# Kernel optimization log

Hardware: AMD Instinct MI355X
Metric: run time of the kernel (lower is better)

The kernel has to match this reference:

```python
import jax, jax.numpy as jnp
import numpy as np

WINDOW = 5  # window_size from init
C_COARSE = 256
C_FINE = 128


def _gather_windows(fine_nchw, b, lin_idx, stride, pad, w, wc):
    """Extract [M, w*w, C] windows centered on coarse grid cells.

    Equivalent to F.unfold(kernel=w, stride=stride, padding=pad) followed by
    rearrange('n (c ww) l -> n l ww c') and fancy-indexing [b, lin_idx],
    but gathers only the matched windows.
    """
    x = jnp.pad(fine_nchw, ((0, 0), (0, 0), (pad, pad), (pad, pad)))
    x = jnp.transpose(x, (0, 2, 3, 1))  # [N, Hp, Wp, C]
    r = lin_idx // wc
    c = lin_idx % wc
    offs = jnp.arange(w)
    rows = r[:, None] * stride + offs  # [M, w] (start = r*stride - pad, +pad shift)
    cols = c[:, None] * stride + offs  # [M, w]
    patches = x[b[:, None, None], rows[:, :, None], cols[:, None, :]]  # [M, w, w, C]
    return patches.reshape(patches.shape[0], w * w, patches.shape[-1])


def setup_inputs() -> dict:
    key = jax.random.key(0)
    ks = jax.random.split(key, 10)
    N, Hc, Hf, M = 2, 60, 240, 3000
    inp = {
        "coarse_image_feature_1": jax.random.normal(ks[0], (N, Hc * Hc, C_COARSE), jnp.float32),
        "coarse_image_feature_2": jax.random.normal(ks[1], (N, Hc * Hc, C_COARSE), jnp.float32),
        "fine_image_feature_1": jax.random.normal(ks[2], (N, C_FINE, Hf, Hf), jnp.float32),
        "fine_image_feature_2": jax.random.normal(ks[3], (N, C_FINE, Hf, Hf), jnp.float32),
        "batch_indices": jax.random.randint(ks[4], (M,), 0, N),
        "row_indices": jax.random.randint(ks[5], (M,), 0, Hc * Hc),
        "column_indices": jax.random.randint(ks[6], (M,), 0, Hc * Hc),
        "fine_height_width": Hf,
        "coarse_height_width": Hc,
        # learned params (kaiming-normal-ish weights, zero biases)
        "W_dp": jax.random.normal(ks[7], (C_FINE, C_COARSE), jnp.float32) * np.sqrt(2.0 / C_FINE),
        "b_dp": jnp.zeros((C_FINE,), jnp.float32),
        "W_merge": jax.random.normal(ks[8], (C_FINE, 2 * C_FINE), jnp.float32) * np.sqrt(2.0 / C_FINE),
        "b_merge": jnp.zeros((C_FINE,), jnp.float32),
    }
    return inp


def reference(coarse_image_feature_1, coarse_image_feature_2,
              fine_image_feature_1, fine_image_feature_2,
              batch_indices, row_indices, column_indices,
              fine_height_width, coarse_height_width,
              W_dp, b_dp, W_merge, b_merge):
    stride = fine_height_width // coarse_height_width
    pad = WINDOW // 2
    M = batch_indices.shape[0]

    f1 = _gather_windows(fine_image_feature_1, batch_indices, row_indices,
                         stride, pad, WINDOW, coarse_height_width)       # [M, ww, Cf]
    f2 = _gather_windows(fine_image_feature_2, batch_indices, column_indices,
                         stride, pad, WINDOW, coarse_height_width)       # [M, ww, Cf]

    coarse = jnp.concatenate([
        coarse_image_feature_1[batch_indices, row_indices],
        coarse_image_feature_2[batch_indices, column_indices],
    ], axis=0)                                                           # [2M, Cc]
    coarse = coarse @ W_dp.T + b_dp                                      # [2M, Cf]

    fine = jnp.concatenate([f1, f2], axis=0)                             # [2M, ww, Cf]
    combined = jnp.concatenate(
        [fine, jnp.broadcast_to(coarse[:, None, :], fine.shape)], axis=-1)  # [2M, ww, 2Cf]
    merged = combined @ W_merge.T + b_merge                              # [2M, ww, Cf]
    return merged[:M], merged[M:]
```

## Files before the change

kernel.cpp:

```cpp
#include <hip/hip_runtime.h>

#define HF 240
#define HC 60
#define STRIDEF 4
#define PADW 2
#define WIN 5
#define CC 256
#define CF 128
#define NPOS 25
#define NPX (HF*HF)
#define MPB 16
#define TPX 128

typedef __bf16 bf16x8 __attribute__((ext_vector_type(8)));
typedef __bf16 bf16x4 __attribute__((ext_vector_type(4)));
typedef float  f32x4  __attribute__((ext_vector_type(4)));

__global__ void k_prep(const float* __restrict__ W_dp, const float* __restrict__ b_dp,
                       const float* __restrict__ W_merge, const float* __restrict__ b_merge,
                       __bf16* __restrict__ Wm1h, float* __restrict__ W_effT,
                       float* __restrict__ b_eff) {
    const int j = blockIdx.x;
    const int k = threadIdx.x;
    const float* wm2 = W_merge + (size_t)j * (2 * CF) + CF;

    float acc = 0.f, accb = 0.f;
    for (int q = 0; q < CF; ++q) {
        const float wq = wm2[q];
        acc  += wq * W_dp[(size_t)q * CC + k];
        accb += wq * b_dp[q];
    }
    W_effT[(size_t)k * CF + j] = acc;

    if (k < CF)
        Wm1h[(size_t)j * CF + k] = (__bf16)W_merge[(size_t)j * (2 * CF) + k];
    if (k == 0)
        b_eff[j] = accb + b_merge[j];
}

__global__ void k_coarse(const float* __restrict__ c1, const float* __restrict__ c2,
                         const int* __restrict__ bidx, const int* __restrict__ ridx,
                         const int* __restrict__ cidx, int M,
                         const float* __restrict__ W_effT, const float* __restrict__ b_eff,
                         float* __restrict__ c_all) {
    const int m0 = blockIdx.x * MPB;
    const int j  = threadIdx.x;
    const int twoM = 2 * M;
    __shared__ float v[MPB * CC];

    const int nm = (twoM - m0) < MPB ? (twoM - m0) : MPB;
    for (int mm = 0; mm < nm; ++mm) {
        int m = m0 + mm;
        const float* src;
        if (m < M) src = c1 + ((size_t)bidx[m] * (HC * HC) + ridx[m]) * CC;
        else       src = c2 + ((size_t)bidx[m - M] * (HC * HC) + cidx[m - M]) * CC;
        v[mm * CC + j]      = src[j];
        v[mm * CC + j + CF] = src[j + CF];
    }
    __syncthreads();

    float acc[MPB];
    const float be = b_eff[j];
    #pragma unroll
    for (int mm = 0; mm < MPB; ++mm) acc[mm] = be;

    for (int k = 0; k < CC; k += 4) {
        float w0 = W_effT[(k + 0) * CF + j];
        float w1 = W_effT[(k + 1) * CF + j];
        float w2 = W_effT[(k + 2) * CF + j];
        float w3 = W_effT[(k + 3) * CF + j];
        #pragma unroll
        for (int mm = 0; mm < MPB; ++mm) {
            const f32x4 vv = *(const f32x4*)&v[mm * CC + k];
            acc[mm] += w0 * vv.x + w1 * vv.y + w2 * vv.z + w3 * vv.w;
        }
    }
    for (int mm = 0; mm < nm; ++mm)
        c_all[(size_t)(m0 + mm) * CF + j] = acc[mm];
}

__global__ __launch_bounds__(256, 4) void k_tgemm(
    const float* __restrict__ f1, const float* __restrict__ f2,
    const __bf16* __restrict__ Wm1h, __bf16* __restrict__ V) {

    const int slot = blockIdx.y;
    const float* src = (slot >= 2 ? f2 : f1) + (size_t)(slot & 1) * CF * NPX;
    const int px0 = blockIdx.x * TPX;
    const int t  = threadIdx.x;
    const int l  = t & 63;
    const int w  = t >> 6;
    const int lo16 = l & 15;
    const int hi   = l >> 4;

    __shared__ __attribute__((aligned(16))) float chkf[2][32 * TPX];

    const int seg = l >> 5;
    const int q4  = (l & 31) * 4;

#define STAGE(c, b)                                                           \
    {                                                                         \
        _Pragma("unroll")                                                     \
        for (int ii = 0; ii < 4; ++ii) {                                      \
            const int i   = w * 4 + ii;                                       \
            const int chl = 2 * i + seg;                                      \
            const int ch  = (c) * 32 + chl;                                   \
            const int pxg = q4 ^ (((ch >> 3) & 3) << 4);                      \
            const float* gp = src + (size_t)ch * NPX + px0 + pxg;             \
            __builtin_amdgcn_global_load_lds(                                 \
                (const __attribute__((address_space(1))) void*)gp,            \
                (__attribute__((address_space(3))) void*)&chkf[b][i * 256],   \
                16, 0, 0);                                                    \
        }                                                                     \
    }

    f32x4 acc[8][2];
    #pragma unroll
    for (int mt = 0; mt < 8; ++mt) {
        acc[mt][0] = (f32x4){0.f, 0.f, 0.f, 0.f};
        acc[mt][1] = (f32x4){0.f, 0.f, 0.f, 0.f};
    }

    STAGE(0, 0);

    #pragma unroll
    for (int c = 0; c < 4; ++c) {
        const int b = c & 1;
        if (c < 3) STAGE(c + 1, b ^ 1);
        __syncthreads();

        const bf16x8 bf0 = *reinterpret_cast<const bf16x8*>(
            Wm1h + (size_t)(w * 32 + 2 * lo16 + 0) * CF + c * 32 + hi * 8);
        const bf16x8 bf1 = *reinterpret_cast<const bf16x8*>(
            Wm1h + (size_t)(w * 32 + 2 * lo16 + 1) * CF + c * 32 + hi * 8);

        #pragma unroll
        for (int mt = 0; mt < 8; ++mt) {
            const int pxr = (mt * 16 + lo16) ^ (hi << 4);
            bf16x8 a;
            #pragma unroll
            for (int e = 0; e < 8; ++e)
                a[e] = (__bf16)chkf[b][(hi * 8 + e) * TPX + pxr];
            acc[mt][0] = __builtin_amdgcn_mfma_f32_16x16x32_bf16(a, bf0, acc[mt][0], 0, 0, 0);
            acc[mt][1] = __builtin_amdgcn_mfma_f32_16x16x32_bf16(a, bf1, acc[mt][1], 0, 0, 0);
        }
        __syncthreads();
    }
#undef STAGE

    uint* Vp = (uint*)(V + ((size_t)slot * NPX + px0) * CF);
    const int dcol = w * 16 + lo16;
    #pragma unroll
    for (int mt = 0; mt < 8; ++mt) {
        #pragma unroll
        for (int reg = 0; reg < 4; ++reg) {
            const int px = mt * 16 + hi * 4 + reg;
            union { uint u; __bf16 h[2]; } cv;
            cv.h[0] = (__bf16)acc[mt][0][reg];
            cv.h[1] = (__bf16)acc[mt][1][reg];
            Vp[(size_t)px * 64 + dcol] = cv.u;
        }
    }
}

__global__ __launch_bounds__(256) void k_gather(
    const __bf16* __restrict__ V,
    const int* __restrict__ bidx, const int* __restrict__ ridx,
    const int* __restrict__ cidx, int M,
    const float* __restrict__ c_all, float* __restrict__ out) {

    const int m = blockIdx.x;
    const int t = threadIdx.x;
    const int g  = t >> 5;
    const int l32 = t & 31;

    int b, lin, ii;
    if (m < M) { ii = 0; b = bidx[m];     lin = ridx[m]; }
    else       { ii = 1; b = bidx[m - M]; lin = cidx[m - M]; }
    const int slot = ii * 2 + b;
    const int r  = lin / HC, c = lin - r * HC;
    const int y0 = r * STRIDEF - PADW;
    const int x0 = c * STRIDEF - PADW;

    const f32x4 c4 = *reinterpret_cast<const f32x4*>(c_all + (size_t)m * CF + l32 * 4);
    const __bf16* Vb = V + (size_t)slot * NPX * CF;
    float* ob = out + (size_t)m * (NPOS * CF) + l32 * 4;

    #pragma unroll
    for (int pass = 0; pass < 4; ++pass) {
        const int p = pass * 8 + g;
        if (p < NPOS) {
            const int wy = (p * 13) >> 6;
            const int wx = p - wy * WIN;
            const int y = y0 + wy, x = x0 + wx;
            f32x4 o = c4;
            if (y >= 0 && x >= 0) {
                const bf16x4 v = *reinterpret_cast<const bf16x4*>(Vb + (size_t)(y * HF + x) * CF + l32 * 4);
                o.x += (float)v.x; o.y += (float)v.y; o.z += (float)v.z; o.w += (float)v.w;
            }
            __builtin_nontemporal_store(o, reinterpret_cast<f32x4*>(ob + (size_t)p * CF));
        }
    }
}

__global__ __launch_bounds__(256) void k_main_direct(
    const float* __restrict__ f1, const float* __restrict__ f2,
    const int* __restrict__ bidx, const int* __restrict__ ridx,
    const int* __restrict__ cidx, int M,
    const __bf16* __restrict__ Wm1h, const float* __restrict__ c_all,
    float* __restrict__ out) {

    const int m = blockIdx.x;
    const int t = threadIdx.x;
    const int l    = t & 63;
    const int wv   = t >> 6;
    const int lo16 = l & 15;
    const int hi   = l >> 4;

    __shared__ __bf16 patch[32 * CF];

    bf16x8 bfrag[2][4];
    #pragma unroll
    for (int nt2 = 0; nt2 < 2; ++nt2) {
        const int j = wv * 32 + nt2 * 16 + lo16;
        #pragma unroll
        for (int kt = 0; kt < 4; ++kt)
            bfrag[nt2][kt] = *reinterpret_cast<const bf16x8*>(Wm1h + (size_t)j * CF + kt * 32 + hi * 8);
    }

    const float* img; int b, lin;
    if (m < M) { img = f1; b = bidx[m];     lin = ridx[m]; }
    else       { img = f2; b = bidx[m - M]; lin = cidx[m - M]; }
    const int r  = lin / HC, c = lin - r * HC;
    const int y0 = r * STRIDEF - PADW;
    const int x0 = c * STRIDEF - PADW;

    for (int task = t; task < CF * WIN; task += 256) {
        const int ch = task / WIN;
        const int wy = task - ch * WIN;
        const int y  = y0 + wy;
        const bool yok = (y >= 0);
        const float* rowp = img + (((size_t)b * CF + ch) * HF + (yok ? y : 0)) * HF;
        #pragma unroll
        for (int wx = 0; wx < WIN; ++wx) {
            const int x = x0 + wx;
            const float val = (yok && x >= 0) ? rowp[x] : 0.f;
            const int pos = wy * WIN + wx;
            patch[pos * CF + (ch ^ ((pos & 7) << 3))] = (__bf16)val;
        }
    }
    __syncthreads();

    f32x4 acc[2][2];
    #pragma unroll
    for (int mt = 0; mt < 2; ++mt)
        #pragma unroll
        for (int nt2 = 0; nt2 < 2; ++nt2)
            acc[mt][nt2] = (f32x4){0.f, 0.f, 0.f, 0.f};

    const int swz = (lo16 & 7) << 3;
    #pragma unroll
    for (int kt = 0; kt < 4; ++kt) {
        const int koff = (kt * 32 + hi * 8) ^ swz;
        bf16x8 a0 = *reinterpret_cast<const bf16x8*>(&patch[ lo16       * CF + koff]);
        bf16x8 a1 = *reinterpret_cast<const bf16x8*>(&patch[(16 + lo16) * CF + koff]);
        #pragma unroll
        for (int nt2 = 0; nt2 < 2; ++nt2) {
            acc[0][nt2] = __builtin_amdgcn_mfma_f32_16x16x32_bf16(a0, bfrag[nt2][kt], acc[0][nt2], 0, 0, 0);
            acc[1][nt2] = __builtin_amdgcn_mfma_f32_16x16x32_bf16(a1, bfrag[nt2][kt], acc[1][nt2], 0, 0, 0);
        }
    }

    float* ob = out + (size_t)m * (NPOS * CF);
    #pragma unroll
    for (int nt2 = 0; nt2 < 2; ++nt2) {
        const int j  = wv * 32 + nt2 * 16 + lo16;
        const float cv = c_all[(size_t)m * CF + j];
        #pragma unroll
        for (int mt = 0; mt < 2; ++mt) {
            #pragma unroll
            for (int reg = 0; reg < 4; ++reg) {
                const int p = mt * 16 + hi * 4 + reg;
                if (p < NPOS)
                    ob[(size_t)p * CF + j] = acc[mt][nt2][reg] + cv;
            }
        }
    }
}

extern "C" void kernel_launch(void* const* d_in, const int* in_sizes, int n_in,
                              void* d_out, int out_size, void* d_ws, size_t ws_size,
                              hipStream_t stream) {
    const float* c1      = (const float*)d_in[0];
    const float* c2      = (const float*)d_in[1];
    const float* f1      = (const float*)d_in[2];
    const float* f2      = (const float*)d_in[3];
    const int*   bidx    = (const int*)d_in[4];
    const int*   ridx    = (const int*)d_in[5];
    const int*   cidx    = (const int*)d_in[6];
    const float* W_dp    = (const float*)d_in[9];
    const float* b_dp    = (const float*)d_in[10];
    const float* W_merge = (const float*)d_in[11];
    const float* b_merge = (const float*)d_in[12];
    const int M = in_sizes[4];

    char* ws = (char*)d_ws;
    __bf16* Wm1h  = (__bf16*)(ws);
    float* W_effT = (float*)(ws + (64 << 10));
    float* b_eff  = (float*)(ws + (192 << 10));
    float* c_all  = (float*)(ws + (256 << 10));
    __bf16* V     = (__bf16*)(ws + (4 << 20));

    const size_t need_V = (size_t)(4 << 20) + (size_t)4 * NPX * CF * 2;

    hipLaunchKernelGGL(k_prep, dim3(CF), dim3(CC), 0, stream,
                       W_dp, b_dp, W_merge, b_merge, Wm1h, W_effT, b_eff);
    hipLaunchKernelGGL(k_coarse, dim3((2 * M + MPB - 1) / MPB), dim3(CF), 0, stream,
                       c1, c2, bidx, ridx, cidx, M, W_effT, b_eff, c_all);

    if (ws_size >= need_V) {
        hipLaunchKernelGGL(k_tgemm, dim3(NPX / TPX, 4), dim3(256), 0, stream,
                           f1, f2, Wm1h, V);
        hipLaunchKernelGGL(k_gather, dim3(2 * M), dim3(256), 0, stream,
                           V, bidx, ridx, cidx, M, c_all, (float*)d_out);
    } else {
        hipLaunchKernelGGL(k_main_direct, dim3(2 * M), dim3(256), 0, stream,
                           f1, f2, bidx, ridx, cidx, M, Wm1h, c_all, (float*)d_out);
    }
}
```

Measured before the change: 92.86 us.

## Widen tgemm pixel tile, drop LDS double buffer, remap slabs per XCD

Doubles the pixel tile of the transform GEMM to 256 pixels per block, so each block keeps 16 MFMA row tiles and reuses each weight fragment across twice as many pixels. The double-buffered LDS staging is replaced by a single buffer that is loaded and then consumed, which removes the load/compute overlap but keeps LDS at the same size. Block indices are remapped so consecutive slabs fall on the same XCD, aiming at better L2 locality. Risks are fewer blocks in flight, more accumulator registers, and exposed load latency.

```diff
diff --git a/kernel.cpp b/kernel.cpp
--- a/kernel.cpp
+++ b/kernel.cpp
@@ -10,7 +10,8 @@
 #define NPOS 25
 #define NPX (HF*HF)
 #define MPB 16
-#define TPX 128
+#define TPX 256
+#define NSLAB (NPX / TPX)
 
 typedef __bf16 bf16x8 __attribute__((ext_vector_type(8)));
 typedef __bf16 bf16x4 __attribute__((ext_vector_type(4)));
@@ -79,78 +80,71 @@
         c_all[(size_t)(m0 + mm) * CF + j] = acc[mm];
 }
 
-__global__ __launch_bounds__(256, 4) void k_tgemm(
+__global__ __launch_bounds__(256, 3) void k_tgemm(
     const float* __restrict__ f1, const float* __restrict__ f2,
     const __bf16* __restrict__ Wm1h, __bf16* __restrict__ V) {
 
+    int slab = blockIdx.x;
+    {
+        const int q = NSLAB / 8, r = NSLAB % 8;
+        const int xcd = slab & 7, off = slab >> 3;
+        slab = (xcd < r ? xcd * (q + 1) : r * (q + 1) + (xcd - r) * q) + off;
+    }
     const int slot = blockIdx.y;
     const float* src = (slot >= 2 ? f2 : f1) + (size_t)(slot & 1) * CF * NPX;
-    const int px0 = blockIdx.x * TPX;
+    const int px0 = slab * TPX;
     const int t  = threadIdx.x;
     const int l  = t & 63;
     const int w  = t >> 6;
     const int lo16 = l & 15;
     const int hi   = l >> 4;
 
-    __shared__ __attribute__((aligned(16))) float chkf[2][32 * TPX];
-
-    const int seg = l >> 5;
-    const int q4  = (l & 31) * 4;
-
-#define STAGE(c, b)                                                           \
-    {                                                                         \
-        _Pragma("unroll")                                                     \
-        for (int ii = 0; ii < 4; ++ii) {                                      \
-            const int i   = w * 4 + ii;                                       \
-            const int chl = 2 * i + seg;                                      \
-            const int ch  = (c) * 32 + chl;                                   \
-            const int pxg = q4 ^ (((ch >> 3) & 3) << 4);                      \
-            const float* gp = src + (size_t)ch * NPX + px0 + pxg;             \
-            __builtin_amdgcn_global_load_lds(                                 \
-                (const __attribute__((address_space(1))) void*)gp,            \
-                (__attribute__((address_space(3))) void*)&chkf[b][i * 256],   \
-                16, 0, 0);                                                    \
-        }                                                                     \
-    }
-
-    f32x4 acc[8][2];
-    #pragma unroll
-    for (int mt = 0; mt < 8; ++mt) {
+    __shared__ __attribute__((aligned(16))) float chkf[32 * TPX];
+
+    f32x4 acc[16][2];
+    #pragma unroll
+    for (int mt = 0; mt < 16; ++mt) {
         acc[mt][0] = (f32x4){0.f, 0.f, 0.f, 0.f};
         acc[mt][1] = (f32x4){0.f, 0.f, 0.f, 0.f};
     }
 
-    STAGE(0, 0);
-
-    #pragma unroll
-    for (int c = 0; c < 4; ++c) {
-        const int b = c & 1;
-        if (c < 3) STAGE(c + 1, b ^ 1);
+    #pragma unroll
+    for (int g = 0; g < 4; ++g) {
+        #pragma unroll
+        for (int ii = 0; ii < 8; ++ii) {
+            const int i  = w * 8 + ii;
+            const int ch = g * 32 + i;
+            const int pxg = (4 * l) ^ (((ch >> 3) & 3) << 4);
+            const float* gp = src + (size_t)ch * NPX + px0 + pxg;
+            __builtin_amdgcn_global_load_lds(
+                (const __attribute__((address_space(1))) void*)gp,
+                (__attribute__((address_space(3))) void*)&chkf[i * TPX],
+                16, 0, 0);
+        }
         __syncthreads();
 
         const bf16x8 bf0 = *reinterpret_cast<const bf16x8*>(
-            Wm1h + (size_t)(w * 32 + 2 * lo16 + 0) * CF + c * 32 + hi * 8);
+            Wm1h + (size_t)(w * 32 + 2 * lo16 + 0) * CF + g * 32 + hi * 8);
         const bf16x8 bf1 = *reinterpret_cast<const bf16x8*>(
-            Wm1h + (size_t)(w * 32 + 2 * lo16 + 1) * CF + c * 32 + hi * 8);
-
-        #pragma unroll
-        for (int mt = 0; mt < 8; ++mt) {
+            Wm1h + (size_t)(w * 32 + 2 * lo16 + 1) * CF + g * 32 + hi * 8);
+
+        #pragma unroll
+        for (int mt = 0; mt < 16; ++mt) {
             const int pxr = (mt * 16 + lo16) ^ (hi << 4);
             bf16x8 a;
             #pragma unroll
             for (int e = 0; e < 8; ++e)
-                a[e] = (__bf16)chkf[b][(hi * 8 + e) * TPX + pxr];
+                a[e] = (__bf16)chkf[(hi * 8 + e) * TPX + pxr];
             acc[mt][0] = __builtin_amdgcn_mfma_f32_16x16x32_bf16(a, bf0, acc[mt][0], 0, 0, 0);
             acc[mt][1] = __builtin_amdgcn_mfma_f32_16x16x32_bf16(a, bf1, acc[mt][1], 0, 0, 0);
         }
         __syncthreads();
     }
-#undef STAGE
 
     uint* Vp = (uint*)(V + ((size_t)slot * NPX + px0) * CF);
     const int dcol = w * 16 + lo16;
     #pragma unroll
-    for (int mt = 0; mt < 8; ++mt) {
+    for (int mt = 0; mt < 16; ++mt) {
         #pragma unroll
         for (int reg = 0; reg < 4; ++reg) {
             const int px = mt * 16 + hi * 4 + reg;
@@ -318,7 +312,7 @@
                        c1, c2, bidx, ridx, cidx, M, W_effT, b_eff, c_all);
 
     if (ws_size >= need_V) {
-        hipLaunchKernelGGL(k_tgemm, dim3(NPX / TPX, 4), dim3(256), 0, stream,
+        hipLaunchKernelGGL(k_tgemm, dim3(NSLAB, 4), dim3(256), 0, stream,
                            f1, f2, Wm1h, V);
         hipLaunchKernelGGL(k_gather, dim3(2 * M), dim3(256), 0, stream,
                            V, bidx, ridx, cidx, M, c_all, (float*)d_out);
```

Measured after the change: 117.8 us. +26.9%, slower.

## Pre-convert fine images to bf16 and stage tiles via global_load_lds

Applied to the files above, without the earlier changes.

Adds a separate pass that converts both fine feature maps from fp32 to bf16 in workspace with nontemporal loads and stores. A new transform GEMM kernel then reads the half-size bf16 tiles straight into LDS through global_load_lds with an XOR swizzle, double-buffered. The aim is to cut GEMM-side load traffic and the in-kernel conversion work. In exchange it adds a full extra read and write pass over both images, plus a kernel launch, and needs a larger workspace (64MB offset) before this path is taken.

```diff
diff --git a/kernel.cpp b/kernel.cpp
--- a/kernel.cpp
+++ b/kernel.cpp
@@ -77,6 +77,102 @@
     }
     for (int mm = 0; mm < nm; ++mm)
         c_all[(size_t)(m0 + mm) * CF + j] = acc[mm];
+}
+
+__global__ __launch_bounds__(256) void k_conv(
+    const float* __restrict__ f1, const float* __restrict__ f2,
+    __bf16* __restrict__ T) {
+    const float* src = blockIdx.y ? f2 : f1;
+    __bf16* dst = T + (size_t)blockIdx.y * 2 * CF * NPX;
+    const size_t n4 = (size_t)2 * CF * NPX / 4;
+    const size_t step = (size_t)gridDim.x * 256;
+    for (size_t i = (size_t)blockIdx.x * 256 + threadIdx.x; i < n4; i += step) {
+        const f32x4 v = __builtin_nontemporal_load((const f32x4*)src + i);
+        bf16x4 o = { (__bf16)v.x, (__bf16)v.y, (__bf16)v.z, (__bf16)v.w };
+        __builtin_nontemporal_store(o, (bf16x4*)dst + i);
+    }
+}
+
+__global__ __launch_bounds__(256, 4) void k_tgemm_h(
+    const __bf16* __restrict__ T,
+    const __bf16* __restrict__ Wm1h, __bf16* __restrict__ V) {
+
+    const int slot = blockIdx.y;
+    const __bf16* src = T + (size_t)slot * CF * NPX;
+    const int px0 = blockIdx.x * TPX;
+    const int t  = threadIdx.x;
+    const int l  = t & 63;
+    const int w  = t >> 6;
+    const int lo16 = l & 15;
+    const int hi   = l >> 4;
+
+    __shared__ __attribute__((aligned(16))) __bf16 chk[2][32 * TPX];
+
+    const int row4 = l >> 4;
+    const int px8  = (l & 15) * 8;
+
+#define STAGE(c, b)                                                           \
+    {                                                                         \
+        _Pragma("unroll")                                                     \
+        for (int ii = 0; ii < 2; ++ii) {                                      \
+            const int i  = w * 2 + ii;                        \
+            const int ch = (c) * 32 + i * 4 + row4;                           \
+            const int pxg = px8 ^ ((((ch) >> 3) & 3) << 4);                   \
+            const __bf16* gp = src + (size_t)ch * NPX + px0 + pxg;            \
+            __builtin_amdgcn_global_load_lds(                                 \
+                (const __attribute__((address_space(1))) void*)gp,            \
+                (__attribute__((address_space(3))) void*)&chk[b][i * 512],    \
+                16, 0, 0);                                                    \
+        }                                                                     \
+    }
+
+    f32x4 acc[8][2];
+    #pragma unroll
+    for (int mt = 0; mt < 8; ++mt) {
+        acc[mt][0] = (f32x4){0.f, 0.f, 0.f, 0.f};
+        acc[mt][1] = (f32x4){0.f, 0.f, 0.f, 0.f};
+    }
+
+    STAGE(0, 0);
+
+    #pragma unroll
+    for (int c = 0; c < 4; ++c) {
+        const int b = c & 1;
+        if (c < 3) STAGE(c + 1, b ^ 1);
+        __syncthreads();
+
+        const bf16x8 bf0 = *reinterpret_cast<const bf16x8*>(
+            Wm1h + (size_t)(w * 32 + 2 * lo16 + 0) * CF + c * 32 + hi * 8);
+        const bf16x8 bf1 = *reinterpret_cast<const bf16x8*>(
+            Wm1h + (size_t)(w * 32 + 2 * lo16 + 1) * CF + c * 32 + hi * 8);
+
+        #pragma unroll
+        for (int mt = 0; mt < 8; ++mt) {
+            const int pxr = (mt * 16 + lo16) ^ (hi << 4);
+            bf16x8 a;
+            #pragma unroll
+            for (int e = 0; e < 8; ++e)
+                a[e] = chk[b][(hi * 8 + e) * TPX + pxr];
+            acc[mt][0] = __builtin_amdgcn_mfma_f32_16x16x32_bf16(a, bf0, acc[mt][0], 0, 0, 0);
+            acc[mt][1] = __builtin_amdgcn_mfma_f32_16x16x32_bf16(a, bf1, acc[mt][1], 0, 0, 0);
+        }
+        __syncthreads();
+    }
+#undef STAGE
+
+    uint* Vp = (uint*)(V + ((size_t)slot * NPX + px0) * CF);
+    const int dcol = w * 16 + lo16;
+    #pragma unroll
+    for (int mt = 0; mt < 8; ++mt) {
+        #pragma unroll
+        for (int reg = 0; reg < 4; ++reg) {
+            const int px = mt * 16 + hi * 4 + reg;
+            union { uint u; __bf16 h[2]; } cv;
+            cv.h[0] = (__bf16)acc[mt][0][reg];
+            cv.h[1] = (__bf16)acc[mt][1][reg];
+            Vp[(size_t)px * 64 + dcol] = cv.u;
+        }
+    }
 }
 
 __global__ __launch_bounds__(256, 4) void k_tgemm(
@@ -309,15 +405,25 @@
     float* b_eff  = (float*)(ws + (192 << 10));
     float* c_all  = (float*)(ws + (256 << 10));
     __bf16* V     = (__bf16*)(ws + (4 << 20));
-
-    const size_t need_V = (size_t)(4 << 20) + (size_t)4 * NPX * CF * 2;
+    __bf16* T     = (__bf16*)(ws + (64 << 20));
+
+    const size_t img_elems = (size_t)4 * NPX * CF;
+    const size_t need_V = (size_t)(4 << 20) + img_elems * 2;
+    const size_t need_T = (size_t)(64 << 20) + img_elems * 2;
 
     hipLaunchKernelGGL(k_prep, dim3(CF), dim3(CC), 0, stream,
                        W_dp, b_dp, W_merge, b_merge, Wm1h, W_effT, b_eff);
     hipLaunchKernelGGL(k_coarse, dim3((2 * M + MPB - 1) / MPB), dim3(CF), 0, stream,
                        c1, c2, bidx, ridx, cidx, M, W_effT, b_eff, c_all);
 
-    if (ws_size >= need_V) {
+    if (ws_size >= need_T) {
+        hipLaunchKernelGGL(k_conv, dim3(1024, 2), dim3(256), 0, stream,
+                           f1, f2, T);
+        hipLaunchKernelGGL(k_tgemm_h, dim3(NPX / TPX, 4), dim3(256), 0, stream,
+                           T, Wm1h, V);
+        hipLaunchKernelGGL(k_gather, dim3(2 * M), dim3(256), 0, stream,
+                           V, bidx, ridx, cidx, M, c_all, (float*)d_out);
+    } else if (ws_size >= need_V) {
         hipLaunchKernelGGL(k_tgemm, dim3(NPX / TPX, 4), dim3(256), 0, stream,
                            f1, f2, Wm1h, V);
         hipLaunchKernelGGL(k_gather, dim3(2 * M), dim3(256), 0, stream,
```

Measured after the change: 120.0 us. +29.2%, slower.
